# Kernel optimization log

Hardware: AMD Instinct MI355X
Metric: run time of the kernel (lower is better)

Reference implementation:

```python
import jax, jax.numpy as jnp
import numpy as np

N_NODES = 10000
N_EDGES = 640000
IN_CH = 128
OUT_CH = 128


def setup_inputs() -> dict:
    key = jax.random.key(0)
    k1, k2, k3, k4 = jax.random.split(key, 4)
    x = jax.random.normal(k1, (N_NODES, IN_CH), dtype=jnp.float32)
    edge_index = jax.random.randint(k2, (2, N_EDGES), 0, N_NODES, dtype=jnp.int64)
    # nn.Linear(2*in_channels, out_channels): weight [out, 2*in], bias [out]
    bound = 1.0 / np.sqrt(2 * IN_CH)
    W = jax.random.uniform(k3, (OUT_CH, 2 * IN_CH), dtype=jnp.float32, minval=-bound, maxval=bound)
    b = jax.random.uniform(k4, (OUT_CH,), dtype=jnp.float32, minval=-bound, maxval=bound)
    return {"x": x, "W": W, "b": b, "edge_index": edge_index}


def reference(x, W, b, edge_index):
    # PyG convention: edge_index[0] = source j, edge_index[1] = target i
    src, dst = edge_index[0], edge_index[1]
    x_i = x[dst]                      # [E, C] target features
    x_j = x[src]                      # [E, C] source features
    feat = jnp.concatenate([x_i, x_j - x_i], axis=-1)  # [E, 2C]
    msg = feat @ W.T + b              # [E, out]
    out = jax.ops.segment_max(msg, dst, num_segments=x.shape[0])  # [N, out]
    # isolated nodes: PyG scatter-max yields 0, segment_max yields -inf
    return jnp.where(jnp.isfinite(out), out, 0.0)
```

## Files before the change

kernel.cpp:

```cpp
#include <hip/hip_runtime.h>
#include <math.h>

#define N_CH 128
#define NB_MAX 1024
#define ECHUNK 2048
#define GCHUNK 2048

__global__ __launch_bounds__(256) void prep_kernel(const float* __restrict__ W,
                                                   float* __restrict__ V1,
                                                   float* __restrict__ V2,
                                                   int* __restrict__ binCount,
                                                   int nb) {
    int i = blockIdx.x * 256 + threadIdx.x;
    if (i < N_CH * N_CH) {
        int k = i >> 7, o = i & 127;
        float w1 = W[o * 256 + k];
        float w2 = W[o * 256 + 128 + k];
        int ip = (k >> 2) * 512 + o * 4 + (k & 3);
        V1[ip] = w1 - w2;
        V2[ip] = w2;
    }
    if (i < nb) binCount[i] = 0;
}

__global__ __launch_bounds__(256) void gemm_kernel(const float* __restrict__ x,
                                                   const float* __restrict__ V1,
                                                   const float* __restrict__ V2,
                                                   const float* __restrict__ bias,
                                                   const int* __restrict__ dst,
                                                   float* __restrict__ A,
                                                   unsigned short* __restrict__ Bh,
                                                   int* __restrict__ binCount,
                                                   int n_nodes, int n_edges, int nb) {
    __shared__ float xs[16][N_CH];
    __shared__ int h[NB_MAX];
    const int tid = threadIdx.x;
    const int bid = blockIdx.x;

    const int ebase = bid * ECHUNK;
    if (ebase < n_edges) {
        const int ecnt = min(ECHUNK, n_edges - ebase);
        for (int i = tid; i < nb; i += 256) h[i] = 0;
        __syncthreads();
        const int j = tid * 8;
        if (j + 8 <= ecnt) {
            int4 d0 = *(const int4*)(dst + ebase + j);
            int4 d1 = *(const int4*)(dst + ebase + j + 4);
            atomicAdd(&h[d0.x >> 4], 1); atomicAdd(&h[d0.y >> 4], 1);
            atomicAdd(&h[d0.z >> 4], 1); atomicAdd(&h[d0.w >> 4], 1);
            atomicAdd(&h[d1.x >> 4], 1); atomicAdd(&h[d1.y >> 4], 1);
            atomicAdd(&h[d1.z >> 4], 1); atomicAdd(&h[d1.w >> 4], 1);
        } else {
            for (int q = j; q < min(j + 8, ecnt); ++q)
                atomicAdd(&h[dst[ebase + q] >> 4], 1);
        }
        __syncthreads();
        for (int i = tid; i < nb; i += 256)
            if (h[i]) atomicAdd(&binCount[i], h[i]);
    }

    const int n0 = bid * 16;
    if (n0 >= n_nodes) return;

    if (n0 + 16 <= n_nodes) {
        const float4* xg = (const float4*)(x + (size_t)n0 * N_CH);
        float4* xsv = (float4*)&xs[0][0];
        xsv[tid] = xg[tid];
        xsv[tid + 256] = xg[tid + 256];
    } else {
        for (int i = tid; i < 16 * N_CH; i += 256) {
            int n = n0 + (i >> 7);
            (&xs[0][0])[i] = (n < n_nodes) ? x[(size_t)n * N_CH + (i & 127)] : 0.f;
        }
    }
    __syncthreads();

    const int o  = tid & 127;
    const int nh = tid >> 7;
    const float bo = bias[o];
    float acc1[8], acc2[8];
    #pragma unroll
    for (int i = 0; i < 8; ++i) { acc1[i] = 0.f; acc2[i] = 0.f; }

    const float* xrow = &xs[nh * 8][0];
    for (int k4 = 0; k4 < N_CH; k4 += 4) {
        float4 w1 = *(const float4*)(V1 + k4 * 128 + o * 4);
        float4 w2 = *(const float4*)(V2 + k4 * 128 + o * 4);
        #pragma unroll
        for (int i = 0; i < 8; ++i) {
            float4 xv = *(const float4*)&xrow[i * N_CH + k4];
            acc1[i] = fmaf(xv.x, w1.x, acc1[i]); acc2[i] = fmaf(xv.x, w2.x, acc2[i]);
            acc1[i] = fmaf(xv.y, w1.y, acc1[i]); acc2[i] = fmaf(xv.y, w2.y, acc2[i]);
            acc1[i] = fmaf(xv.z, w1.z, acc1[i]); acc2[i] = fmaf(xv.z, w2.z, acc2[i]);
            acc1[i] = fmaf(xv.w, w1.w, acc1[i]); acc2[i] = fmaf(xv.w, w2.w, acc2[i]);
        }
    }

    #pragma unroll
    for (int i = 0; i < 8; ++i) {
        int n = n0 + nh * 8 + i;
        if (n < n_nodes) {
            A[(size_t)n * N_CH + o] = acc1[i] + bo;
            unsigned int bits = __float_as_uint(acc2[i]);
            unsigned int r = (bits + 0x7FFFu + ((bits >> 16) & 1u)) >> 16;
            Bh[(size_t)n * N_CH + o] = (unsigned short)r;
        }
    }
}

__global__ __launch_bounds__(1024) void scan_kernel(const int* __restrict__ binCount,
                                                    int* __restrict__ binOffG,
                                                    int* __restrict__ binCursor,
                                                    int nb) {
    __shared__ int sc[1024];
    const int tid = threadIdx.x;
    int c = (tid < nb) ? binCount[tid] : 0;
    int p = (c + 3) & ~3;
    sc[tid] = p;
    __syncthreads();
    #pragma unroll
    for (int off = 1; off < 1024; off <<= 1) {
        int u = (tid >= off) ? sc[tid - off] : 0;
        __syncthreads();
        sc[tid] += u;
        __syncthreads();
    }
    if (tid < nb) {
        int excl = sc[tid] - p;
        binOffG[tid] = excl;
        binCursor[tid] = excl;
    }
}

__global__ __launch_bounds__(256) void bin_kernel(const int* __restrict__ src,
                                                  const int* __restrict__ dst,
                                                  int* __restrict__ binCursor,
                                                  unsigned int* __restrict__ binned,
                                                  int n_edges, int nb) {
    __shared__ int hist[NB_MAX];
    __shared__ int rbase[NB_MAX];
    const int tid = threadIdx.x;
    const int base = blockIdx.x * ECHUNK;
    const int cnt = min(ECHUNK, n_edges - base);

    for (int i = tid; i < nb; i += 256) hist[i] = 0;
    __syncthreads();

    const int j = tid * 8;
    const int mc = max(0, min(8, cnt - j));
    unsigned int pk[8]; int bb[8], rr[8];
    if (mc == 8) {
        int4 s0 = *(const int4*)(src + base + j);
        int4 s1 = *(const int4*)(src + base + j + 4);
        int4 d0 = *(const int4*)(dst + base + j);
        int4 d1 = *(const int4*)(dst + base + j + 4);
        int sv[8] = {s0.x, s0.y, s0.z, s0.w, s1.x, s1.y, s1.z, s1.w};
        int dv[8] = {d0.x, d0.y, d0.z, d0.w, d1.x, d1.y, d1.z, d1.w};
        #pragma unroll
        for (int k = 0; k < 8; ++k) {
            int b = dv[k] >> 4;
            pk[k] = ((unsigned int)(dv[k] & 15) << 14) | (unsigned int)sv[k];
            bb[k] = b;
            rr[k] = atomicAdd(&hist[b], 1);
        }
    } else {
        for (int k = 0; k < mc; ++k) {
            int sv = src[base + j + k];
            int dv = dst[base + j + k];
            int b = dv >> 4;
            pk[k] = ((unsigned int)(dv & 15) << 14) | (unsigned int)sv;
            bb[k] = b;
            rr[k] = atomicAdd(&hist[b], 1);
        }
    }
    __syncthreads();

    for (int i = tid; i < nb; i += 256) {
        int c = hist[i];
        if (c) rbase[i] = atomicAdd(&binCursor[i], c);
    }
    __syncthreads();

    for (int k = 0; k < mc; ++k)
        binned[rbase[bb[k]] + rr[k]] = pk[k];
}

#define FOLD4(acc_lo, acc_hi, a, b, c, d)                                        \
    acc_lo = fmaxf(acc_lo, fmaxf(fmaxf(__uint_as_float((a) << 16),               \
                                       __uint_as_float((b) << 16)),              \
                                 fmaxf(__uint_as_float((c) << 16),               \
                                       __uint_as_float((d) << 16))));            \
    acc_hi = fmaxf(acc_hi, fmaxf(fmaxf(__uint_as_float((a) & 0xFFFF0000u),       \
                                       __uint_as_float((b) & 0xFFFF0000u)),      \
                                 fmaxf(__uint_as_float((c) & 0xFFFF0000u),       \
                                       __uint_as_float((d) & 0xFFFF0000u))));

__global__ __launch_bounds__(256) void gather_kernel(
        const float* __restrict__ A,
        const uint4* __restrict__ Bh4,
        const int* __restrict__ binOffG,
        const int* __restrict__ binCount,
        const unsigned int* __restrict__ binned,
        float* __restrict__ out,
        int n_nodes) {
    __shared__ int lidx[GCHUNK];
    __shared__ int h16[16], e17[17];
    const int b = blockIdx.x;
    const int tid = threadIdx.x;
    const int wv  = tid >> 6;
    const int l   = tid & 63;
    const int sub = l >> 4;
    const int col = l & 15;
    const int rbeg = binOffG[b];
    const int cnt  = binCount[b];

    float mlo[4][4], mhi[4][4]; int tcnt[4];
    #pragma unroll
    for (int i = 0; i < 4; ++i) {
        tcnt[i] = 0;
        #pragma unroll
        for (int u = 0; u < 4; ++u) { mlo[i][u] = -INFINITY; mhi[i][u] = -INFINITY; }
    }

    for (int cb = 0; cb < cnt; cb += GCHUNK) {
        const int ccnt = min(GCHUNK, cnt - cb);
        if (tid < 16) h16[tid] = 0;
        __syncthreads();

        const int mb = tid * 8;
        const int mc = max(0, min(8, ccnt - mb));
        int myd[8], mys[8], myr[8];
        if (mc == 8) {
            int4 r0 = *(const int4*)((const int*)binned + rbeg + cb + mb);
            int4 r1 = *(const int4*)((const int*)binned + rbeg + cb + mb + 4);
            unsigned int wv8[8] = {(unsigned int)r0.x, (unsigned int)r0.y,
                                   (unsigned int)r0.z, (unsigned int)r0.w,
                                   (unsigned int)r1.x, (unsigned int)r1.y,
                                   (unsigned int)r1.z, (unsigned int)r1.w};
            #pragma unroll
            for (int k = 0; k < 8; ++k) {
                myd[k] = (int)(wv8[k] >> 14);
                mys[k] = (int)(wv8[k] & 16383u);
                myr[k] = atomicAdd(&h16[myd[k]], 1);
            }
        } else {
            for (int k = 0; k < mc; ++k) {
                unsigned int w = binned[rbeg + cb + mb + k];
                myd[k] = (int)(w >> 14);
                mys[k] = (int)(w & 16383u);
                myr[k] = atomicAdd(&h16[myd[k]], 1);
            }
        }
        __syncthreads();
        if (tid == 0) {
            int s = 0;
            #pragma unroll
            for (int k = 0; k < 16; ++k) { e17[k] = s; s += h16[k]; }
            e17[16] = s;
        }
        __syncthreads();
        for (int k = 0; k < mc; ++k)
            lidx[e17[myd[k]] + myr[k]] = mys[k];
        __syncthreads();

        #pragma unroll
        for (int i = 0; i < 4; ++i) {
            const int nl = wv * 4 + i;
            const int c  = h16[nl];
            const int bg = e17[nl];
            tcnt[i] += c;
            int q = 0;
            for (; q + 16 <= c; q += 16) {
                int e0 = lidx[bg + q + sub];
                int e1 = lidx[bg + q + 4 + sub];
                int e2 = lidx[bg + q + 8 + sub];
                int e3 = lidx[bg + q + 12 + sub];
                uint4 w0 = Bh4[(size_t)e0 * 16 + col];
                uint4 w1 = Bh4[(size_t)e1 * 16 + col];
                uint4 w2 = Bh4[(size_t)e2 * 16 + col];
                uint4 w3 = Bh4[(size_t)e3 * 16 + col];
                FOLD4(mlo[i][0], mhi[i][0], w0.x, w1.x, w2.x, w3.x);
                FOLD4(mlo[i][1], mhi[i][1], w0.y, w1.y, w2.y, w3.y);
                FOLD4(mlo[i][2], mhi[i][2], w0.z, w1.z, w2.z, w3.z);
                FOLD4(mlo[i][3], mhi[i][3], w0.w, w1.w, w2.w, w3.w);
            }
            for (; q < c; q += 4) {
                int r = q + sub;
                if (r < c) {
                    uint4 w = Bh4[(size_t)lidx[bg + r] * 16 + col];
                    mlo[i][0] = fmaxf(mlo[i][0], __uint_as_float(w.x << 16));
                    mhi[i][0] = fmaxf(mhi[i][0], __uint_as_float(w.x & 0xFFFF0000u));
                    mlo[i][1] = fmaxf(mlo[i][1], __uint_as_float(w.y << 16));
                    mhi[i][1] = fmaxf(mhi[i][1], __uint_as_float(w.y & 0xFFFF0000u));
                    mlo[i][2] = fmaxf(mlo[i][2], __uint_as_float(w.z << 16));
                    mhi[i][2] = fmaxf(mhi[i][2], __uint_as_float(w.z & 0xFFFF0000u));
                    mlo[i][3] = fmaxf(mlo[i][3], __uint_as_float(w.w << 16));
                    mhi[i][3] = fmaxf(mhi[i][3], __uint_as_float(w.w & 0xFFFF0000u));
                }
            }
        }
        __syncthreads();
    }

    #pragma unroll
    for (int i = 0; i < 4; ++i) {
        const int n = b * 16 + wv * 4 + i;
        if (n >= n_nodes) continue;
        float lo[4], hi[4];
        #pragma unroll
        for (int u = 0; u < 4; ++u) {
            lo[u] = mlo[i][u]; hi[u] = mhi[i][u];
            lo[u] = fmaxf(lo[u], __shfl_xor(lo[u], 16, 64));
            hi[u] = fmaxf(hi[u], __shfl_xor(hi[u], 16, 64));
            lo[u] = fmaxf(lo[u], __shfl_xor(lo[u], 32, 64));
            hi[u] = fmaxf(hi[u], __shfl_xor(hi[u], 32, 64));
        }
        if (sub == 0) {
            float r8[8];
            if (tcnt[i] > 0) {
                const float4* Arow = (const float4*)(A + (size_t)n * N_CH + col * 8);
                float4 a0 = Arow[0], a1 = Arow[1];
                r8[0] = a0.x + lo[0]; r8[1] = a0.y + hi[0];
                r8[2] = a0.z + lo[1]; r8[3] = a0.w + hi[1];
                r8[4] = a1.x + lo[2]; r8[5] = a1.y + hi[2];
                r8[6] = a1.z + lo[3]; r8[7] = a1.w + hi[3];
            } else {
                #pragma unroll
                for (int j2 = 0; j2 < 8; ++j2) r8[j2] = 0.f;
            }
            float4* orow = (float4*)(out + (size_t)n * N_CH + col * 8);
            orow[0] = make_float4(r8[0], r8[1], r8[2], r8[3]);
            orow[1] = make_float4(r8[4], r8[5], r8[6], r8[7]);
        }
    }
}

extern "C" void kernel_launch(void* const* d_in, const int* in_sizes, int n_in,
                              void* d_out, int out_size, void* d_ws, size_t ws_size,
                              hipStream_t stream) {
    const float* x = (const float*)d_in[0];
    const float* W = (const float*)d_in[1];
    const float* b = (const float*)d_in[2];
    const int*   ei = (const int*)d_in[3];

    const int n_nodes = in_sizes[0] / N_CH;
    const int n_edges = in_sizes[3] / 2;
    const int nb = (n_nodes + 15) >> 4;
    const int* src = ei;
    const int* dst = ei + n_edges;
    float* out = (float*)d_out;

    char* ws = (char*)d_ws;
    size_t off = 0;
    auto alloc = [&](size_t bytes) -> void* {
        void* p = ws + off;
        off += (bytes + 255) & ~(size_t)255;
        return p;
    };
    float* V1        = (float*)alloc((size_t)N_CH * N_CH * 4);
    float* V2        = (float*)alloc((size_t)N_CH * N_CH * 4);
    float* A         = (float*)alloc((size_t)n_nodes * N_CH * 4);
    unsigned short* Bh = (unsigned short*)alloc((size_t)n_nodes * N_CH * 2);
    int*   binCount  = (int*)alloc((size_t)nb * 4);
    int*   binCursor = (int*)alloc((size_t)nb * 4);
    int*   binOffG   = (int*)alloc((size_t)nb * 4);
    unsigned int* binned = (unsigned int*)alloc(((size_t)n_edges + 4 * NB_MAX) * 4);
    (void)ws_size; (void)n_in; (void)out_size;

    const int nodeChunks = (n_nodes + 15) >> 4;
    const int edgeChunks = (n_edges + ECHUNK - 1) / ECHUNK;
    const int ng = max(nodeChunks, edgeChunks);

    prep_kernel  <<<64, 256, 0, stream>>>(W, V1, V2, binCount, nb);
    gemm_kernel  <<<ng, 256, 0, stream>>>(x, V1, V2, b, dst, A, Bh, binCount,
                                          n_nodes, n_edges, nb);
    scan_kernel  <<<1, 1024, 0, stream>>>(binCount, binOffG, binCursor, nb);
    bin_kernel   <<<edgeChunks, 256, 0, stream>>>(src, dst, binCursor, binned,
                                                  n_edges, nb);
    gather_kernel<<<nb, 256, 0, stream>>>(A, (const uint4*)Bh, binOffG, binCount,
                                          binned, out, n_nodes);
}
```

Baseline: 128.2 us.

## Use bf16 MFMA for node GEMM and deepen gather unroll to 32 edges

The per-node fp32 FMA GEMM is replaced by bf16 MFMA 16x16x32 instructions. x tiles are converted to bf16 in padded shared memory, and the weight matrices are pre-converted to bf16 in row-major layout. The gather loop gains a 32-edge unrolled path that issues 8 independent loads per lane to raise memory-level parallelism. Rounding inputs and weights to bf16 lowers accuracy of the A term, which was previously fp32.

```diff
diff --git a/kernel.cpp b/kernel.cpp
--- a/kernel.cpp
+++ b/kernel.cpp
@@ -5,34 +5,44 @@
 #define NB_MAX 1024
 #define ECHUNK 2048
 #define GCHUNK 2048
+#define XPAD 8
+#define XLD (N_CH + XPAD)
+
+typedef __attribute__((ext_vector_type(8))) short bf16x8;
+typedef __attribute__((ext_vector_type(4))) float f32x4;
+
+__device__ __forceinline__ unsigned short f2bf(float f) {
+    unsigned int bits = __float_as_uint(f);
+    unsigned int r = (bits + 0x7FFFu + ((bits >> 16) & 1u)) >> 16;
+    return (unsigned short)r;
+}
 
 __global__ __launch_bounds__(256) void prep_kernel(const float* __restrict__ W,
-                                                   float* __restrict__ V1,
-                                                   float* __restrict__ V2,
+                                                   unsigned short* __restrict__ V1b,
+                                                   unsigned short* __restrict__ V2b,
                                                    int* __restrict__ binCount,
                                                    int nb) {
     int i = blockIdx.x * 256 + threadIdx.x;
     if (i < N_CH * N_CH) {
-        int k = i >> 7, o = i & 127;
+        int o = i >> 7, k = i & 127;
         float w1 = W[o * 256 + k];
         float w2 = W[o * 256 + 128 + k];
-        int ip = (k >> 2) * 512 + o * 4 + (k & 3);
-        V1[ip] = w1 - w2;
-        V2[ip] = w2;
+        V1b[i] = f2bf(w1 - w2);
+        V2b[i] = f2bf(w2);
     }
     if (i < nb) binCount[i] = 0;
 }
 
 __global__ __launch_bounds__(256) void gemm_kernel(const float* __restrict__ x,
-                                                   const float* __restrict__ V1,
-                                                   const float* __restrict__ V2,
+                                                   const unsigned short* __restrict__ V1b,
+                                                   const unsigned short* __restrict__ V2b,
                                                    const float* __restrict__ bias,
                                                    const int* __restrict__ dst,
                                                    float* __restrict__ A,
                                                    unsigned short* __restrict__ Bh,
                                                    int* __restrict__ binCount,
                                                    int n_nodes, int n_edges, int nb) {
-    __shared__ float xs[16][N_CH];
+    __shared__ unsigned short xs[16][XLD];
     __shared__ int h[NB_MAX];
     const int tid = threadIdx.x;
     const int bid = blockIdx.x;
@@ -64,46 +74,64 @@
 
     if (n0 + 16 <= n_nodes) {
         const float4* xg = (const float4*)(x + (size_t)n0 * N_CH);
-        float4* xsv = (float4*)&xs[0][0];
-        xsv[tid] = xg[tid];
-        xsv[tid + 256] = xg[tid + 256];
+        #pragma unroll
+        for (int i = 0; i < 2; ++i) {
+            int f = tid + i * 256;
+            float4 v = xg[f];
+            int row = f >> 5, c4 = (f & 31) * 4;
+            unsigned short* p = &xs[row][c4];
+            p[0] = f2bf(v.x); p[1] = f2bf(v.y); p[2] = f2bf(v.z); p[3] = f2bf(v.w);
+        }
     } else {
         for (int i = tid; i < 16 * N_CH; i += 256) {
             int n = n0 + (i >> 7);
-            (&xs[0][0])[i] = (n < n_nodes) ? x[(size_t)n * N_CH + (i & 127)] : 0.f;
+            xs[i >> 7][i & 127] = (n < n_nodes) ? f2bf(x[(size_t)n * N_CH + (i & 127)])
+                                                : (unsigned short)0;
         }
     }
     __syncthreads();
 
-    const int o  = tid & 127;
-    const int nh = tid >> 7;
-    const float bo = bias[o];
-    float acc1[8], acc2[8];
-    #pragma unroll
-    for (int i = 0; i < 8; ++i) { acc1[i] = 0.f; acc2[i] = 0.f; }
-
-    const float* xrow = &xs[nh * 8][0];
-    for (int k4 = 0; k4 < N_CH; k4 += 4) {
-        float4 w1 = *(const float4*)(V1 + k4 * 128 + o * 4);
-        float4 w2 = *(const float4*)(V2 + k4 * 128 + o * 4);
-        #pragma unroll
-        for (int i = 0; i < 8; ++i) {
-            float4 xv = *(const float4*)&xrow[i * N_CH + k4];
-            acc1[i] = fmaf(xv.x, w1.x, acc1[i]); acc2[i] = fmaf(xv.x, w2.x, acc2[i]);
-            acc1[i] = fmaf(xv.y, w1.y, acc1[i]); acc2[i] = fmaf(xv.y, w2.y, acc2[i]);
-            acc1[i] = fmaf(xv.z, w1.z, acc1[i]); acc2[i] = fmaf(xv.z, w2.z, acc2[i]);
-            acc1[i] = fmaf(xv.w, w1.w, acc1[i]); acc2[i] = fmaf(xv.w, w2.w, acc2[i]);
-        }
-    }
-
-    #pragma unroll
-    for (int i = 0; i < 8; ++i) {
-        int n = n0 + nh * 8 + i;
-        if (n < n_nodes) {
-            A[(size_t)n * N_CH + o] = acc1[i] + bo;
-            unsigned int bits = __float_as_uint(acc2[i]);
-            unsigned int r = (bits + 0x7FFFu + ((bits >> 16) & 1u)) >> 16;
-            Bh[(size_t)n * N_CH + o] = (unsigned short)r;
+    const int w  = tid >> 6;
+    const int l  = tid & 63;
+    const int lc = l & 15;
+    const int lk = (l >> 4) * 8;
+
+    const int obase = w * 32;
+    bf16x8 b1[2][4], b2[2][4];
+    #pragma unroll
+    for (int t = 0; t < 2; ++t) {
+        const int o = obase + t * 16 + lc;
+        #pragma unroll
+        for (int kb = 0; kb < 4; ++kb) {
+            b1[t][kb] = *(const bf16x8*)(V1b + o * 128 + kb * 32 + lk);
+            b2[t][kb] = *(const bf16x8*)(V2b + o * 128 + kb * 32 + lk);
+        }
+    }
+
+    f32x4 c1[2] = {{0.f,0.f,0.f,0.f},{0.f,0.f,0.f,0.f}};
+    f32x4 c2[2] = {{0.f,0.f,0.f,0.f},{0.f,0.f,0.f,0.f}};
+    #pragma unroll
+    for (int kb = 0; kb < 4; ++kb) {
+        bf16x8 a = *(const bf16x8*)(&xs[lc][kb * 32 + lk]);
+        #pragma unroll
+        for (int t = 0; t < 2; ++t) {
+            c1[t] = __builtin_amdgcn_mfma_f32_16x16x32_bf16(a, b1[t][kb], c1[t], 0, 0, 0);
+            c2[t] = __builtin_amdgcn_mfma_f32_16x16x32_bf16(a, b2[t][kb], c2[t], 0, 0, 0);
+        }
+    }
+
+    const int nrow0 = (l >> 4) * 4;
+    #pragma unroll
+    for (int t = 0; t < 2; ++t) {
+        const int o = obase + t * 16 + lc;
+        const float bo = bias[o];
+        #pragma unroll
+        for (int r = 0; r < 4; ++r) {
+            const int n = n0 + nrow0 + r;
+            if (n < n_nodes) {
+                A[(size_t)n * N_CH + o] = c1[t][r] + bo;
+                Bh[(size_t)n * N_CH + o] = f2bf(c2[t][r]);
+            }
         }
     }
 }
@@ -270,6 +298,22 @@
             const int bg = e17[nl];
             tcnt[i] += c;
             int q = 0;
+            for (; q + 32 <= c; q += 32) {
+                int e[8];
+                #pragma unroll
+                for (int s = 0; s < 8; ++s) e[s] = lidx[bg + q + 4 * s + sub];
+                uint4 w[8];
+                #pragma unroll
+                for (int s = 0; s < 8; ++s) w[s] = Bh4[(size_t)e[s] * 16 + col];
+                FOLD4(mlo[i][0], mhi[i][0], w[0].x, w[1].x, w[2].x, w[3].x);
+                FOLD4(mlo[i][1], mhi[i][1], w[0].y, w[1].y, w[2].y, w[3].y);
+                FOLD4(mlo[i][2], mhi[i][2], w[0].z, w[1].z, w[2].z, w[3].z);
+                FOLD4(mlo[i][3], mhi[i][3], w[0].w, w[1].w, w[2].w, w[3].w);
+                FOLD4(mlo[i][0], mhi[i][0], w[4].x, w[5].x, w[6].x, w[7].x);
+                FOLD4(mlo[i][1], mhi[i][1], w[4].y, w[5].y, w[6].y, w[7].y);
+                FOLD4(mlo[i][2], mhi[i][2], w[4].z, w[5].z, w[6].z, w[7].z);
+                FOLD4(mlo[i][3], mhi[i][3], w[4].w, w[5].w, w[6].w, w[7].w);
+            }
             for (; q + 16 <= c; q += 16) {
                 int e0 = lidx[bg + q + sub];
                 int e1 = lidx[bg + q + 4 + sub];
@@ -357,8 +401,8 @@
         off += (bytes + 255) & ~(size_t)255;
         return p;
     };
-    float* V1        = (float*)alloc((size_t)N_CH * N_CH * 4);
-    float* V2        = (float*)alloc((size_t)N_CH * N_CH * 4);
+    unsigned short* V1b = (unsigned short*)alloc((size_t)N_CH * N_CH * 2);
+    unsigned short* V2b = (unsigned short*)alloc((size_t)N_CH * N_CH * 2);
     float* A         = (float*)alloc((size_t)n_nodes * N_CH * 4);
     unsigned short* Bh = (unsigned short*)alloc((size_t)n_nodes * N_CH * 2);
     int*   binCount  = (int*)alloc((size_t)nb * 4);
@@ -371,8 +415,8 @@
     const int edgeChunks = (n_edges + ECHUNK - 1) / ECHUNK;
     const int ng = max(nodeChunks, edgeChunks);
 
-    prep_kernel  <<<64, 256, 0, stream>>>(W, V1, V2, binCount, nb);
-    gemm_kernel  <<<ng, 256, 0, stream>>>(x, V1, V2, b, dst, A, Bh, binCount,
+    prep_kernel  <<<64, 256, 0, stream>>>(W, V1b, V2b, binCount, nb);
+    gemm_kernel  <<<ng, 256, 0, stream>>>(x, V1b, V2b, b, dst, A, Bh, binCount,
                                           n_nodes, n_edges, nb);
     scan_kernel  <<<1, 1024, 0, stream>>>(binCount, binOffG, binCursor, nb);
     bin_kernel   <<<edgeChunks, 256, 0, stream>>>(src, dst, binCursor, binned,
```

After: 117.3 us (median of 2 runs). 1.09x faster.
